# Kernel tuning notes

Hardware: AMD Instinct MI355X
Metric: run time of the kernel (lower is better)

Reference implementation:

```python
import jax, jax.numpy as jnp
import numpy as np

D = 64      # n_embd (== head_size in this module)
H = 8       # n_heads
B = 4
T = 2048    # seq len == block_size
EPS = 1e-5


def layernorm(x, g, b):
    mu = jnp.mean(x, axis=-1, keepdims=True)
    var = jnp.mean(jnp.square(x - mu), axis=-1, keepdims=True)
    return (x - mu) * jax.lax.rsqrt(var + EPS) * g + b


def setup_inputs() -> dict:
    key = jax.random.key(0)
    ks = jax.random.split(key, 16)
    s = 1.0 / np.sqrt(D)
    inp = {
        'inputs': jax.random.normal(ks[0], (B, T, D), jnp.float32),
        # per-head QKV linears: weight [H, D, D] (in, out), bias [H, D]
        'Wq': jax.random.uniform(ks[1], (H, D, D), jnp.float32, -s, s),
        'bq': jax.random.uniform(ks[2], (H, D), jnp.float32, -s, s),
        'Wk': jax.random.uniform(ks[3], (H, D, D), jnp.float32, -s, s),
        'bk': jax.random.uniform(ks[4], (H, D), jnp.float32, -s, s),
        'Wv': jax.random.uniform(ks[5], (H, D, D), jnp.float32, -s, s),
        'bv': jax.random.uniform(ks[6], (H, D), jnp.float32, -s, s),
        # projection: Linear(H*D -> D)
        'Wp': jax.random.uniform(ks[7], (H * D, D), jnp.float32, -1/np.sqrt(H*D), 1/np.sqrt(H*D)),
        'bp': jax.random.uniform(ks[8], (D,), jnp.float32, -1/np.sqrt(H*D), 1/np.sqrt(H*D)),
        # FFN: D -> 4D -> D
        'W1': jax.random.uniform(ks[9], (D, 4 * D), jnp.float32, -s, s),
        'b1': jax.random.uniform(ks[10], (4 * D,), jnp.float32, -s, s),
        'W2': jax.random.uniform(ks[11], (4 * D, D), jnp.float32, -1/np.sqrt(4*D), 1/np.sqrt(4*D)),
        'b2': jax.random.uniform(ks[12], (D,), jnp.float32, -1/np.sqrt(4*D), 1/np.sqrt(4*D)),
        'g1': jnp.ones((D,), jnp.float32), 'be1': jnp.zeros((D,), jnp.float32),
        'g2': jnp.ones((D,), jnp.float32), 'be2': jnp.zeros((D,), jnp.float32),
    }
    return inp


def reference(inputs, Wq, bq, Wk, bk, Wv, bv, Wp, bp, W1, b1, W2, b2, g1, be1, g2, be2):
    x = inputs
    # per-head full-width QKV: [H, B, T, D]
    q = jnp.einsum('btd,hde->hbte', x, Wq) + bq[:, None, None, :]
    k = jnp.einsum('btd,hde->hbte', x, Wk) + bk[:, None, None, :]
    v = jnp.einsum('btd,hde->hbte', x, Wv) + bv[:, None, None, :]
    # unscaled scores (module has no 1/sqrt(d) scaling)
    scores = jnp.einsum('hbte,hbse->hbts', q, k)  # [H, B, T, T]
    causal = jnp.tril(jnp.ones((T, T), bool))
    scores = jnp.where(causal, scores, -jnp.inf)
    attn = jax.nn.softmax(scores, axis=-1)
    out = jnp.einsum('hbts,hbse->hbte', attn, v)  # [H, B, T, D]
    # torch.cat over heads along last dim -> [B, T, H*D]
    cat = jnp.transpose(out, (1, 2, 0, 3)).reshape(B, T, H * D)
    attn_out = cat @ Wp + bp
    h1 = layernorm(x + attn_out, g1, be1)
    ffn = jax.nn.relu(h1 @ W1 + b1) @ W2 + b2
    return layernorm(h1 + ffn, g2, be2)
```

## Files before the change

### kernel.cpp

```cpp
#include <hip/hip_runtime.h>
#include <hip/hip_bf16.h>
#include <stdint.h>

#define Dd 64
#define Hh 8
#define Bb 4
#define Tt 2048
#define NT (Bb * Tt)

typedef __attribute__((ext_vector_type(4))) float f32x4;
typedef __attribute__((ext_vector_type(8))) __bf16 bf16x8;
typedef __attribute__((ext_vector_type(8))) uint16_t u16x8;

__device__ __forceinline__ uint16_t f2bf_fast(float f) {
    union { __bf16 h; uint16_t u; } c; c.h = (__bf16)f; return c.u;
}

#define SWZ(row, k)   ((row) * 72  + ((k) ^ ((((row) >> 3) & 7) << 3)))
#define PSZ(q, k)     ((q)  * 72  + ((k) ^ ((((q)  >> 2) & 3) << 3)))
#define W2SWZ(col, k) ((col) * 264 + ((k) ^ ((((col) >> 3) & 7) << 3)))
#define WPSWZ(col, k) ((col) * 520 + ((k) ^ ((((col) >> 3) & 7) << 3)))

__global__ __launch_bounds__(256) void qkv_kernel(
    const float* __restrict__ x,
    const float* __restrict__ Wq, const float* __restrict__ bq,
    const float* __restrict__ Wk, const float* __restrict__ bk,
    const float* __restrict__ Wv, const float* __restrict__ bv,
    uint16_t* __restrict__ qb, uint16_t* __restrict__ kb, uint16_t* __restrict__ vb)
{
    __shared__ uint16_t WtF[64 * 72];
    const int rt = blockIdx.x, h = blockIdx.y, m = blockIdx.z;
    const float* W    = (m == 0) ? Wq : (m == 1) ? Wk : Wv;
    const float* bias = (m == 0) ? bq : (m == 1) ? bk : bv;
    uint16_t*    out  = (m == 0) ? qb : (m == 1) ? kb : vb;
    const int t = threadIdx.x, lane = t & 63, w = t >> 6;
    const int l15 = lane & 15, g = lane >> 4;

#pragma unroll
    for (int p = 0; p < 4; ++p) {
        int idx = p * 256 + t;
        int r = idx >> 4, c4 = (idx & 15) * 4;
        f32x4 wv = *(const f32x4*)&W[(size_t)(h * 64 + r) * 64 + c4];
#pragma unroll
        for (int j = 0; j < 4; ++j) WtF[SWZ(c4 + j, r)] = f2bf_fast(wv[j]);
    }

    const int row = rt * 64 + w * 16 + l15;
    union { u16x8 u; bf16x8 b; } a0, a1;
    {
        f32x4 x0 = *(const f32x4*)&x[(size_t)row * 64 + g * 8];
        f32x4 x1 = *(const f32x4*)&x[(size_t)row * 64 + g * 8 + 4];
        f32x4 x2 = *(const f32x4*)&x[(size_t)row * 64 + 32 + g * 8];
        f32x4 x3 = *(const f32x4*)&x[(size_t)row * 64 + 32 + g * 8 + 4];
#pragma unroll
        for (int j = 0; j < 4; ++j) {
            a0.u[j] = f2bf_fast(x0[j]); a0.u[4 + j] = f2bf_fast(x1[j]);
            a1.u[j] = f2bf_fast(x2[j]); a1.u[4 + j] = f2bf_fast(x3[j]);
        }
    }
    __syncthreads();

    f32x4 acc[4] = {};
#pragma unroll
    for (int ct = 0; ct < 4; ++ct) {
        bf16x8 b0 = *(const bf16x8*)&WtF[SWZ(ct * 16 + l15, g * 8)];
        bf16x8 b1 = *(const bf16x8*)&WtF[SWZ(ct * 16 + l15, 32 + g * 8)];
        acc[ct] = __builtin_amdgcn_mfma_f32_16x16x32_bf16(a0.b, b0, acc[ct], 0, 0, 0);
        acc[ct] = __builtin_amdgcn_mfma_f32_16x16x32_bf16(a1.b, b1, acc[ct], 0, 0, 0);
    }
#pragma unroll
    for (int ct = 0; ct < 4; ++ct) {
        float bb = bias[h * 64 + ct * 16 + l15];
#pragma unroll
        for (int rr = 0; rr < 4; ++rr) {
            int orow = rt * 64 + w * 16 + g * 4 + rr;
            out[((size_t)h * NT + orow) * 64 + ct * 16 + l15] =
                f2bf_fast(acc[ct][rr] + bb);
        }
    }
}

__global__ __launch_bounds__(256) void attn_kernel3(
    const uint16_t* __restrict__ qb, const uint16_t* __restrict__ kb,
    const uint16_t* __restrict__ vb, uint16_t* __restrict__ cat)
{
    __shared__ uint16_t KsF[2][64 * 72];
    __shared__ uint16_t VtF[2][64 * 72];
    __shared__ uint16_t PsF[4][16 * 72];
    const int pairid = blockIdx.x, h = blockIdx.y, b = blockIdx.z;
    const int t = threadIdx.x, lane = t & 63, wave = t >> 6;
    const int l15 = lane & 15, g = lane >> 4;
    const size_t base = ((size_t)h * NT + (size_t)b * Tt) * 64;
    const uint16_t* Qh = qb + base;
    const uint16_t* Kh = kb + base;
    const uint16_t* Vh = vb + base;
    const int rS = t >> 3, cS = (t & 7) * 8;

    for (int ph = 0; ph < 2; ++ph) {
        const int qt = ph ? (31 - pairid) : pairid;
        bf16x8 aq0, aq1;
        {
            int qrow = qt * 64 + wave * 16 + l15;
            aq0 = *(const bf16x8*)&Qh[(size_t)qrow * 64 + g * 8];
            aq1 = *(const bf16x8*)&Qh[(size_t)qrow * 64 + 32 + g * 8];
        }
        f32x4 o[4] = {};
        float m_run[4], l_run[4];
#pragma unroll
        for (int r = 0; r < 4; ++r) { m_run[r] = -INFINITY; l_run[r] = 0.f; }

        __syncthreads();
        {
            u16x8 k0 = *(const u16x8*)&Kh[(size_t)(rS) * 64 + cS];
            u16x8 k1 = *(const u16x8*)&Kh[(size_t)(32 + rS) * 64 + cS];
            u16x8 v0 = *(const u16x8*)&Vh[(size_t)(rS) * 64 + cS];
            u16x8 v1 = *(const u16x8*)&Vh[(size_t)(32 + rS) * 64 + cS];
            *(u16x8*)&KsF[0][SWZ(rS, cS)] = k0;
            *(u16x8*)&KsF[0][SWZ(32 + rS, cS)] = k1;
#pragma unroll
            for (int j = 0; j < 8; ++j) {
                VtF[0][SWZ(cS + j, rS)] = v0[j];
                VtF[0][SWZ(cS + j, 32 + rS)] = v1[j];
            }
        }
        __syncthreads();

        for (int kv = 0; kv <= qt; ++kv) {
            const int cur = kv & 1;
            const bool pf = kv < qt;
            u16x8 pk0, pk1, pv0, pv1;
            if (pf) {
                int kr = (kv + 1) * 64;
                pk0 = *(const u16x8*)&Kh[(size_t)(kr + rS) * 64 + cS];
                pk1 = *(const u16x8*)&Kh[(size_t)(kr + 32 + rS) * 64 + cS];
                pv0 = *(const u16x8*)&Vh[(size_t)(kr + rS) * 64 + cS];
                pv1 = *(const u16x8*)&Vh[(size_t)(kr + 32 + rS) * 64 + cS];
            }
            f32x4 s[4];
#pragma unroll
            for (int kt = 0; kt < 4; ++kt) {
                bf16x8 bk0 = *(const bf16x8*)&KsF[cur][SWZ(kt * 16 + l15, g * 8)];
                bf16x8 bk1 = *(const bf16x8*)&KsF[cur][SWZ(kt * 16 + l15, 32 + g * 8)];
                f32x4 z = {};
                z = __builtin_amdgcn_mfma_f32_16x16x32_bf16(aq0, bk0, z, 0, 0, 0);
                z = __builtin_amdgcn_mfma_f32_16x16x32_bf16(aq1, bk1, z, 0, 0, 0);
                s[kt] = z;
            }
            if (kv == qt) {
#pragma unroll
                for (int kt = 0; kt < 4; ++kt) {
                    int key = kt * 16 + l15;
#pragma unroll
                    for (int r = 0; r < 4; ++r) {
                        int qr = wave * 16 + g * 4 + r;
                        if (key > qr) s[kt][r] = -INFINITY;
                    }
                }
            }
            float mt[4];
#pragma unroll
            for (int r = 0; r < 4; ++r) {
                mt[r] = fmaxf(fmaxf(s[0][r], s[1][r]), fmaxf(s[2][r], s[3][r]));
                mt[r] = fmaxf(mt[r], __shfl_xor(mt[r], 1));
                mt[r] = fmaxf(mt[r], __shfl_xor(mt[r], 2));
                mt[r] = fmaxf(mt[r], __shfl_xor(mt[r], 4));
                mt[r] = fmaxf(mt[r], __shfl_xor(mt[r], 8));
            }
            bool need = false;
#pragma unroll
            for (int r = 0; r < 4; ++r) need |= (mt[r] > m_run[r] + 8.f);
            if (__any((int)need)) {
#pragma unroll
                for (int r = 0; r < 4; ++r) {
                    float mnew = fmaxf(m_run[r], mt[r]);
                    float a = __expf(m_run[r] - mnew);
                    m_run[r] = mnew;
                    l_run[r] *= a;
                    o[0][r] *= a; o[1][r] *= a; o[2][r] *= a; o[3][r] *= a;
                }
            }
            float ls[4];
#pragma unroll
            for (int r = 0; r < 4; ++r) {
                float sum = 0.f;
#pragma unroll
                for (int kt = 0; kt < 4; ++kt) {
                    float p = __expf(s[kt][r] - m_run[r]);
                    s[kt][r] = p;
                    sum += p;
                }
                ls[r] = sum;
            }
#pragma unroll
            for (int r = 0; r < 4; ++r) {
                ls[r] += __shfl_xor(ls[r], 1);
                ls[r] += __shfl_xor(ls[r], 2);
                ls[r] += __shfl_xor(ls[r], 4);
                ls[r] += __shfl_xor(ls[r], 8);
                l_run[r] += ls[r];
            }
#pragma unroll
            for (int kt = 0; kt < 4; ++kt)
#pragma unroll
                for (int r = 0; r < 4; ++r)
                    PsF[wave][PSZ(g * 4 + r, kt * 16 + l15)] = f2bf_fast(s[kt][r]);
#pragma unroll
            for (int c = 0; c < 2; ++c) {
                bf16x8 ap = *(const bf16x8*)&PsF[wave][PSZ(l15, c * 32 + g * 8)];
#pragma unroll
                for (int dt = 0; dt < 4; ++dt) {
                    bf16x8 bv = *(const bf16x8*)&VtF[cur][SWZ(dt * 16 + l15, c * 32 + g * 8)];
                    o[dt] = __builtin_amdgcn_mfma_f32_16x16x32_bf16(ap, bv, o[dt], 0, 0, 0);
                }
            }
            if (pf) {
                *(u16x8*)&KsF[cur ^ 1][SWZ(rS, cS)] = pk0;
                *(u16x8*)&KsF[cur ^ 1][SWZ(32 + rS, cS)] = pk1;
#pragma unroll
                for (int j = 0; j < 8; ++j) {
                    VtF[cur ^ 1][SWZ(cS + j, rS)] = pv0[j];
                    VtF[cur ^ 1][SWZ(cS + j, 32 + rS)] = pv1[j];
                }
                __syncthreads();
            }
        }
        float inv[4];
#pragma unroll
        for (int r = 0; r < 4; ++r) inv[r] = 1.f / l_run[r];
#pragma unroll
        for (int dt = 0; dt < 4; ++dt)
#pragma unroll
            for (int r = 0; r < 4; ++r) {
                int row = qt * 64 + wave * 16 + g * 4 + r;
                cat[((size_t)b * Tt + row) * (Hh * 64) + h * 64 + dt * 16 + l15] =
                    f2bf_fast(o[dt][r] * inv[r]);
            }
    }
}

__global__ __launch_bounds__(256) void proj_ln1_mfma(
    const uint16_t* __restrict__ cat, const float* __restrict__ Wp,
    const float* __restrict__ bp, const float* __restrict__ x,
    const float* __restrict__ g1, const float* __restrict__ be1,
    float* __restrict__ h1, uint16_t* __restrict__ h1b)
{
    __shared__ uint16_t WptF[64 * 520];
    const int rt = blockIdx.x;
    const int t = threadIdx.x, lane = t & 63, w = t >> 6;
    const int l15 = lane & 15, g = lane >> 4;
#pragma unroll
    for (int p = 0; p < 32; ++p) {
        int idx = p * 256 + t;
        int r = idx >> 4, c4 = (idx & 15) * 4;
        f32x4 wv = *(const f32x4*)&Wp[(size_t)r * 64 + c4];
#pragma unroll
        for (int j = 0; j < 4; ++j) WptF[WPSWZ(c4 + j, r)] = f2bf_fast(wv[j]);
    }
    __syncthreads();
    const int arow = rt * 64 + w * 16 + l15;
    f32x4 acc[4] = {};
#pragma unroll
    for (int kt = 0; kt < 16; ++kt) {
        bf16x8 a = *(const bf16x8*)&cat[(size_t)arow * 512 + kt * 32 + g * 8];
#pragma unroll
        for (int ct = 0; ct < 4; ++ct) {
            bf16x8 bfr = *(const bf16x8*)&WptF[WPSWZ(ct * 16 + l15, kt * 32 + g * 8)];
            acc[ct] = __builtin_amdgcn_mfma_f32_16x16x32_bf16(a, bfr, acc[ct], 0, 0, 0);
        }
    }
    float bpv[4], g1v[4], b1v[4];
#pragma unroll
    for (int ct = 0; ct < 4; ++ct) {
        bpv[ct] = bp[ct * 16 + l15];
        g1v[ct] = g1[ct * 16 + l15];
        b1v[ct] = be1[ct * 16 + l15];
    }
#pragma unroll
    for (int rr = 0; rr < 4; ++rr) {
        int drow = rt * 64 + w * 16 + g * 4 + rr;
        float s[4], sum = 0.f;
#pragma unroll
        for (int ct = 0; ct < 4; ++ct) {
            s[ct] = acc[ct][rr] + bpv[ct] + x[(size_t)drow * 64 + ct * 16 + l15];
            sum += s[ct];
        }
        sum += __shfl_xor(sum, 1); sum += __shfl_xor(sum, 2);
        sum += __shfl_xor(sum, 4); sum += __shfl_xor(sum, 8);
        float mu = sum * (1.f / 64.f);
        float v = 0.f;
#pragma unroll
        for (int ct = 0; ct < 4; ++ct) { s[ct] -= mu; v += s[ct] * s[ct]; }
        v += __shfl_xor(v, 1); v += __shfl_xor(v, 2);
        v += __shfl_xor(v, 4); v += __shfl_xor(v, 8);
        float rstd = rsqrtf(v * (1.f / 64.f) + 1e-5f);
#pragma unroll
        for (int ct = 0; ct < 4; ++ct) {
            float hv = s[ct] * rstd * g1v[ct] + b1v[ct];
            h1 [(size_t)drow * 64 + ct * 16 + l15] = hv;
            h1b[(size_t)drow * 64 + ct * 16 + l15] = f2bf_fast(hv);
        }
    }
}

__global__ __launch_bounds__(256) void ffn_mfma(
    const uint16_t* __restrict__ h1b, const float* __restrict__ h1,
    const float* __restrict__ W1, const float* __restrict__ b1,
    const float* __restrict__ W2, const float* __restrict__ b2,
    const float* __restrict__ g2, const float* __restrict__ be2,
    float* __restrict__ out)
{
    __shared__ uint16_t W1t[256 * 72];
    __shared__ uint16_t W2t[64 * 264];
    __shared__ uint16_t hidS[4][16 * 264];
    const int rt = blockIdx.x;
    const int t = threadIdx.x, lane = t & 63, w = t >> 6;
    const int l15 = lane & 15, g = lane >> 4;
#pragma unroll
    for (int p = 0; p < 16; ++p) {
        int idx = p * 256 + t;
        int r = idx >> 6, c4 = (idx & 63) * 4;
        f32x4 wv = *(const f32x4*)&W1[(size_t)r * 256 + c4];
#pragma unroll
        for (int j = 0; j < 4; ++j) W1t[SWZ(c4 + j, r)] = f2bf_fast(wv[j]);
    }
#pragma unroll
    for (int p = 0; p < 16; ++p) {
        int idx = p * 256 + t;
        int r = idx >> 4, c4 = (idx & 15) * 4;
        f32x4 wv = *(const f32x4*)&W2[(size_t)r * 64 + c4];
#pragma unroll
        for (int j = 0; j < 4; ++j) W2t[W2SWZ(c4 + j, r)] = f2bf_fast(wv[j]);
    }
    __syncthreads();
    const int arow = rt * 64 + w * 16 + l15;
    f32x4 acc1[16] = {};
#pragma unroll
    for (int ks = 0; ks < 2; ++ks) {
        bf16x8 a = *(const bf16x8*)&h1b[(size_t)arow * 64 + ks * 32 + g * 8];
#pragma unroll
        for (int ct = 0; ct < 16; ++ct) {
            bf16x8 bfr = *(const bf16x8*)&W1t[SWZ(ct * 16 + l15, ks * 32 + g * 8)];
            acc1[ct] = __builtin_amdgcn_mfma_f32_16x16x32_bf16(a, bfr, acc1[ct], 0, 0, 0);
        }
    }
#pragma unroll
    for (int ct = 0; ct < 16; ++ct) {
        float bb = b1[ct * 16 + l15];
#pragma unroll
        for (int rr = 0; rr < 4; ++rr)
            hidS[w][(g * 4 + rr) * 264 + ct * 16 + l15] =
                f2bf_fast(fmaxf(acc1[ct][rr] + bb, 0.f));
    }
    f32x4 acc2[4] = {};
#pragma unroll
    for (int ks = 0; ks < 8; ++ks) {
        bf16x8 a = *(const bf16x8*)&hidS[w][l15 * 264 + ks * 32 + g * 8];
#pragma unroll
        for (int ct = 0; ct < 4; ++ct) {
            bf16x8 bfr = *(const bf16x8*)&W2t[W2SWZ(ct * 16 + l15, ks * 32 + g * 8)];
            acc2[ct] = __builtin_amdgcn_mfma_f32_16x16x32_bf16(a, bfr, acc2[ct], 0, 0, 0);
        }
    }
    float b2v[4], g2v[4], be2v[4];
#pragma unroll
    for (int ct = 0; ct < 4; ++ct) {
        b2v[ct]  = b2[ct * 16 + l15];
        g2v[ct]  = g2[ct * 16 + l15];
        be2v[ct] = be2[ct * 16 + l15];
    }
#pragma unroll
    for (int rr = 0; rr < 4; ++rr) {
        int drow = rt * 64 + w * 16 + g * 4 + rr;
        float s[4], sum = 0.f;
#pragma unroll
        for (int ct = 0; ct < 4; ++ct) {
            s[ct] = acc2[ct][rr] + b2v[ct] + h1[(size_t)drow * 64 + ct * 16 + l15];
            sum += s[ct];
        }
        sum += __shfl_xor(sum, 1); sum += __shfl_xor(sum, 2);
        sum += __shfl_xor(sum, 4); sum += __shfl_xor(sum, 8);
        float mu = sum * (1.f / 64.f);
        float v = 0.f;
#pragma unroll
        for (int ct = 0; ct < 4; ++ct) { s[ct] -= mu; v += s[ct] * s[ct]; }
        v += __shfl_xor(v, 1); v += __shfl_xor(v, 2);
        v += __shfl_xor(v, 4); v += __shfl_xor(v, 8);
        float rstd = rsqrtf(v * (1.f / 64.f) + 1e-5f);
#pragma unroll
        for (int ct = 0; ct < 4; ++ct)
            out[(size_t)drow * 64 + ct * 16 + l15] =
                s[ct] * rstd * g2v[ct] + be2v[ct];
    }
}

extern "C" void kernel_launch(void* const* d_in, const int* in_sizes, int n_in,
                              void* d_out, int out_size, void* d_ws, size_t ws_size,
                              hipStream_t stream)
{
    (void)in_sizes; (void)n_in; (void)out_size; (void)ws_size;
    const float* x   = (const float*)d_in[0];
    const float* Wq  = (const float*)d_in[1];
    const float* bq  = (const float*)d_in[2];
    const float* Wk  = (const float*)d_in[3];
    const float* bk  = (const float*)d_in[4];
    const float* Wv  = (const float*)d_in[5];
    const float* bv  = (const float*)d_in[6];
    const float* Wp  = (const float*)d_in[7];
    const float* bp  = (const float*)d_in[8];
    const float* W1  = (const float*)d_in[9];
    const float* b1  = (const float*)d_in[10];
    const float* W2  = (const float*)d_in[11];
    const float* b2  = (const float*)d_in[12];
    const float* g1  = (const float*)d_in[13];
    const float* be1 = (const float*)d_in[14];
    const float* g2  = (const float*)d_in[15];
    const float* be2 = (const float*)d_in[16];
    float* outp = (float*)d_out;

    char* w = (char*)d_ws;
    uint16_t* qb  = (uint16_t*)w;
    uint16_t* kb  = qb + (size_t)Hh * NT * 64;
    uint16_t* vb  = kb + (size_t)Hh * NT * 64;
    uint16_t* cat = vb + (size_t)Hh * NT * 64;
    float*    h1  = (float*)(cat + (size_t)NT * 512);
    uint16_t* h1b = (uint16_t*)(h1 + (size_t)NT * 64);

    qkv_kernel<<<dim3(NT / 64, Hh, 3), dim3(256), 0, stream>>>(
        x, Wq, bq, Wk, bk, Wv, bv, qb, kb, vb);
    attn_kernel3<<<dim3(16, Hh, Bb), dim3(256), 0, stream>>>(qb, kb, vb, cat);
    proj_ln1_mfma<<<dim3(NT / 64), dim3(256), 0, stream>>>(
        cat, Wp, bp, x, g1, be1, h1, h1b);
    ffn_mfma<<<dim3(NT / 64), dim3(256), 0, stream>>>(
        h1b, h1, W1, b1, W2, b2, g2, be2, outp);
}
```

Before: 192.2 us.

## Pre-convert weights and input to swizzled bf16 once; remap attention grid

Adds a setup kernel that converts x and all weight matrices to bf16 in their swizzled shared-memory layouts once per call. The qkv, projection and FFN kernels then copy those layouts straight into LDS instead of each block re-reading fp32 weights and converting them with scattered stores. The attention launch moves to a 1-D grid with a remapped block index, likely meant to spread heads and batches across XCDs for better L2 locality. This adds one extra kernel launch and extra workspace traffic.

```diff
diff --git a/kernel.cpp b/kernel.cpp
--- a/kernel.cpp
+++ b/kernel.cpp
@@ -21,43 +21,86 @@
 #define W2SWZ(col, k) ((col) * 264 + ((k) ^ ((((col) >> 3) & 7) << 3)))
 #define WPSWZ(col, k) ((col) * 520 + ((k) ^ ((((col) >> 3) & 7) << 3)))
 
+__global__ __launch_bounds__(256) void setup_kernel(
+    const float* __restrict__ x,
+    const float* __restrict__ Wq, const float* __restrict__ Wk,
+    const float* __restrict__ Wv, const float* __restrict__ Wp,
+    const float* __restrict__ W1, const float* __restrict__ W2,
+    uint16_t* __restrict__ xb, uint16_t* __restrict__ WtAll,
+    uint16_t* __restrict__ WptS, uint16_t* __restrict__ W1g,
+    uint16_t* __restrict__ W2g)
+{
+    const int bid = blockIdx.x, t = threadIdx.x;
+    if (bid < 256) {
+        size_t base = ((size_t)bid * 256 + t) * 8;
+        f32x4 a = *(const f32x4*)&x[base];
+        f32x4 b = *(const f32x4*)&x[base + 4];
+        u16x8 o;
+#pragma unroll
+        for (int j = 0; j < 4; ++j) { o[j] = f2bf_fast(a[j]); o[4 + j] = f2bf_fast(b[j]); }
+        *(u16x8*)&xb[base] = o;
+    } else if (bid < 280) {
+        const int mh = bid - 256, m = mh / 8, h = mh % 8;
+        const float* W = (m == 0) ? Wq : (m == 1) ? Wk : Wv;
+        uint16_t* dst = WtAll + (size_t)mh * 4608;
+#pragma unroll
+        for (int p = 0; p < 4; ++p) {
+            int idx = p * 256 + t;
+            int k = idx >> 4, c4 = (idx & 15) * 4;
+            f32x4 wv = *(const f32x4*)&W[(size_t)(h * 64 + k) * 64 + c4];
+#pragma unroll
+            for (int j = 0; j < 4; ++j) dst[SWZ(c4 + j, k)] = f2bf_fast(wv[j]);
+        }
+    } else if (bid < 288) {
+        const int j = bid - 280;
+#pragma unroll
+        for (int p = 0; p < 16; ++p) {
+            int idx = p * 256 + t;
+            int col = idx & 63, k = j * 64 + (idx >> 6);
+            WptS[WPSWZ(col, k)] = f2bf_fast(Wp[(size_t)k * 64 + col]);
+        }
+    } else if (bid < 292) {
+        const int j = bid - 288;
+#pragma unroll
+        for (int p = 0; p < 16; ++p) {
+            int e = j * 4096 + p * 256 + t;
+            int col = e & 255, k = e >> 8;
+            W1g[SWZ(col, k)] = f2bf_fast(W1[(size_t)k * 256 + col]);
+        }
+    } else {
+        const int j = bid - 292;
+#pragma unroll
+        for (int p = 0; p < 16; ++p) {
+            int e = j * 4096 + p * 256 + t;
+            int col = e & 63, k = e >> 6;
+            W2g[W2SWZ(col, k)] = f2bf_fast(W2[(size_t)k * 64 + col]);
+        }
+    }
+}
+
 __global__ __launch_bounds__(256) void qkv_kernel(
-    const float* __restrict__ x,
-    const float* __restrict__ Wq, const float* __restrict__ bq,
-    const float* __restrict__ Wk, const float* __restrict__ bk,
-    const float* __restrict__ Wv, const float* __restrict__ bv,
+    const uint16_t* __restrict__ xb, const uint16_t* __restrict__ WtAll,
+    const float* __restrict__ bq, const float* __restrict__ bk,
+    const float* __restrict__ bv,
     uint16_t* __restrict__ qb, uint16_t* __restrict__ kb, uint16_t* __restrict__ vb)
 {
     __shared__ uint16_t WtF[64 * 72];
     const int rt = blockIdx.x, h = blockIdx.y, m = blockIdx.z;
-    const float* W    = (m == 0) ? Wq : (m == 1) ? Wk : Wv;
     const float* bias = (m == 0) ? bq : (m == 1) ? bk : bv;
     uint16_t*    out  = (m == 0) ? qb : (m == 1) ? kb : vb;
     const int t = threadIdx.x, lane = t & 63, w = t >> 6;
     const int l15 = lane & 15, g = lane >> 4;
 
-#pragma unroll
-    for (int p = 0; p < 4; ++p) {
-        int idx = p * 256 + t;
-        int r = idx >> 4, c4 = (idx & 15) * 4;
-        f32x4 wv = *(const f32x4*)&W[(size_t)(h * 64 + r) * 64 + c4];
-#pragma unroll
-        for (int j = 0; j < 4; ++j) WtF[SWZ(c4 + j, r)] = f2bf_fast(wv[j]);
-    }
-
+    {
+        const u16x8* src = (const u16x8*)(WtAll + (size_t)(m * 8 + h) * 4608);
+        u16x8* dst = (u16x8*)WtF;
+        dst[t] = src[t];
+        dst[256 + t] = src[256 + t];
+        if (t < 64) dst[512 + t] = src[512 + t];
+    }
     const int row = rt * 64 + w * 16 + l15;
-    union { u16x8 u; bf16x8 b; } a0, a1;
-    {
-        f32x4 x0 = *(const f32x4*)&x[(size_t)row * 64 + g * 8];
-        f32x4 x1 = *(const f32x4*)&x[(size_t)row * 64 + g * 8 + 4];
-        f32x4 x2 = *(const f32x4*)&x[(size_t)row * 64 + 32 + g * 8];
-        f32x4 x3 = *(const f32x4*)&x[(size_t)row * 64 + 32 + g * 8 + 4];
-#pragma unroll
-        for (int j = 0; j < 4; ++j) {
-            a0.u[j] = f2bf_fast(x0[j]); a0.u[4 + j] = f2bf_fast(x1[j]);
-            a1.u[j] = f2bf_fast(x2[j]); a1.u[4 + j] = f2bf_fast(x3[j]);
-        }
-    }
+    bf16x8 a0 = *(const bf16x8*)&xb[(size_t)row * 64 + g * 8];
+    bf16x8 a1 = *(const bf16x8*)&xb[(size_t)row * 64 + 32 + g * 8];
     __syncthreads();
 
     f32x4 acc[4] = {};
@@ -65,8 +108,8 @@
     for (int ct = 0; ct < 4; ++ct) {
         bf16x8 b0 = *(const bf16x8*)&WtF[SWZ(ct * 16 + l15, g * 8)];
         bf16x8 b1 = *(const bf16x8*)&WtF[SWZ(ct * 16 + l15, 32 + g * 8)];
-        acc[ct] = __builtin_amdgcn_mfma_f32_16x16x32_bf16(a0.b, b0, acc[ct], 0, 0, 0);
-        acc[ct] = __builtin_amdgcn_mfma_f32_16x16x32_bf16(a1.b, b1, acc[ct], 0, 0, 0);
+        acc[ct] = __builtin_amdgcn_mfma_f32_16x16x32_bf16(a0, b0, acc[ct], 0, 0, 0);
+        acc[ct] = __builtin_amdgcn_mfma_f32_16x16x32_bf16(a1, b1, acc[ct], 0, 0, 0);
     }
 #pragma unroll
     for (int ct = 0; ct < 4; ++ct) {
@@ -80,14 +123,18 @@
     }
 }
 
-__global__ __launch_bounds__(256) void attn_kernel3(
+__global__ __launch_bounds__(256) void attn_kernel4(
     const uint16_t* __restrict__ qb, const uint16_t* __restrict__ kb,
     const uint16_t* __restrict__ vb, uint16_t* __restrict__ cat)
 {
     __shared__ uint16_t KsF[2][64 * 72];
     __shared__ uint16_t VtF[2][64 * 72];
     __shared__ uint16_t PsF[4][16 * 72];
-    const int pairid = blockIdx.x, h = blockIdx.y, b = blockIdx.z;
+    const int bid = blockIdx.x;
+    const int lbid = (bid & 7) * 64 + (bid >> 3);
+    const int pairid = lbid & 15;
+    const int hb = lbid >> 4;
+    const int h = hb & 7, b = hb >> 3;
     const int t = threadIdx.x, lane = t & 63, wave = t >> 6;
     const int l15 = lane & 15, g = lane >> 4;
     const size_t base = ((size_t)h * NT + (size_t)b * Tt) * 64;
@@ -239,7 +286,7 @@
 }
 
 __global__ __launch_bounds__(256) void proj_ln1_mfma(
-    const uint16_t* __restrict__ cat, const float* __restrict__ Wp,
+    const uint16_t* __restrict__ cat, const uint16_t* __restrict__ WptS,
     const float* __restrict__ bp, const float* __restrict__ x,
     const float* __restrict__ g1, const float* __restrict__ be1,
     float* __restrict__ h1, uint16_t* __restrict__ h1b)
@@ -248,13 +295,12 @@
     const int rt = blockIdx.x;
     const int t = threadIdx.x, lane = t & 63, w = t >> 6;
     const int l15 = lane & 15, g = lane >> 4;
-#pragma unroll
-    for (int p = 0; p < 32; ++p) {
-        int idx = p * 256 + t;
-        int r = idx >> 4, c4 = (idx & 15) * 4;
-        f32x4 wv = *(const f32x4*)&Wp[(size_t)r * 64 + c4];
-#pragma unroll
-        for (int j = 0; j < 4; ++j) WptF[WPSWZ(c4 + j, r)] = f2bf_fast(wv[j]);
+    {
+        const u16x8* src = (const u16x8*)WptS;
+        u16x8* dst = (u16x8*)WptF;
+#pragma unroll
+        for (int p = 0; p < 16; ++p) dst[p * 256 + t] = src[p * 256 + t];
+        if (t < 64) dst[4096 + t] = src[4096 + t];
     }
     __syncthreads();
     const int arow = rt * 64 + w * 16 + l15;
@@ -304,32 +350,27 @@
 
 __global__ __launch_bounds__(256) void ffn_mfma(
     const uint16_t* __restrict__ h1b, const float* __restrict__ h1,
-    const float* __restrict__ W1, const float* __restrict__ b1,
-    const float* __restrict__ W2, const float* __restrict__ b2,
+    const uint16_t* __restrict__ w1g, const float* __restrict__ b1,
+    const uint16_t* __restrict__ w2g, const float* __restrict__ b2,
     const float* __restrict__ g2, const float* __restrict__ be2,
     float* __restrict__ out)
 {
-    __shared__ uint16_t W1t[256 * 72];
-    __shared__ uint16_t W2t[64 * 264];
+    __shared__ uint16_t W1s[256 * 72];
+    __shared__ uint16_t W2s[64 * 264];
     __shared__ uint16_t hidS[4][16 * 264];
     const int rt = blockIdx.x;
     const int t = threadIdx.x, lane = t & 63, w = t >> 6;
     const int l15 = lane & 15, g = lane >> 4;
-#pragma unroll
-    for (int p = 0; p < 16; ++p) {
-        int idx = p * 256 + t;
-        int r = idx >> 6, c4 = (idx & 63) * 4;
-        f32x4 wv = *(const f32x4*)&W1[(size_t)r * 256 + c4];
-#pragma unroll
-        for (int j = 0; j < 4; ++j) W1t[SWZ(c4 + j, r)] = f2bf_fast(wv[j]);
-    }
-#pragma unroll
-    for (int p = 0; p < 16; ++p) {
-        int idx = p * 256 + t;
-        int r = idx >> 4, c4 = (idx & 15) * 4;
-        f32x4 wv = *(const f32x4*)&W2[(size_t)r * 64 + c4];
-#pragma unroll
-        for (int j = 0; j < 4; ++j) W2t[W2SWZ(c4 + j, r)] = f2bf_fast(wv[j]);
+    {
+        const u16x8* s1 = (const u16x8*)w1g;
+        u16x8* d1 = (u16x8*)W1s;
+#pragma unroll
+        for (int p = 0; p < 9; ++p) d1[p * 256 + t] = s1[p * 256 + t];
+        const u16x8* s2 = (const u16x8*)w2g;
+        u16x8* d2 = (u16x8*)W2s;
+#pragma unroll
+        for (int p = 0; p < 8; ++p) d2[p * 256 + t] = s2[p * 256 + t];
+        if (t < 64) d2[2048 + t] = s2[2048 + t];
     }
     __syncthreads();
     const int arow = rt * 64 + w * 16 + l15;
@@ -339,7 +380,7 @@
         bf16x8 a = *(const bf16x8*)&h1b[(size_t)arow * 64 + ks * 32 + g * 8];
 #pragma unroll
         for (int ct = 0; ct < 16; ++ct) {
-            bf16x8 bfr = *(const bf16x8*)&W1t[SWZ(ct * 16 + l15, ks * 32 + g * 8)];
+            bf16x8 bfr = *(const bf16x8*)&W1s[SWZ(ct * 16 + l15, ks * 32 + g * 8)];
             acc1[ct] = __builtin_amdgcn_mfma_f32_16x16x32_bf16(a, bfr, acc1[ct], 0, 0, 0);
         }
     }
@@ -357,7 +398,7 @@
         bf16x8 a = *(const bf16x8*)&hidS[w][l15 * 264 + ks * 32 + g * 8];
 #pragma unroll
         for (int ct = 0; ct < 4; ++ct) {
-            bf16x8 bfr = *(const bf16x8*)&W2t[W2SWZ(ct * 16 + l15, ks * 32 + g * 8)];
+            bf16x8 bfr = *(const bf16x8*)&W2s[W2SWZ(ct * 16 + l15, ks * 32 + g * 8)];
             acc2[ct] = __builtin_amdgcn_mfma_f32_16x16x32_bf16(a, bfr, acc2[ct], 0, 0, 0);
         }
     }
@@ -418,18 +459,25 @@
     float* outp = (float*)d_out;
 
     char* w = (char*)d_ws;
-    uint16_t* qb  = (uint16_t*)w;
-    uint16_t* kb  = qb + (size_t)Hh * NT * 64;
-    uint16_t* vb  = kb + (size_t)Hh * NT * 64;
-    uint16_t* cat = vb + (size_t)Hh * NT * 64;
-    float*    h1  = (float*)(cat + (size_t)NT * 512);
-    uint16_t* h1b = (uint16_t*)(h1 + (size_t)NT * 64);
-
+    uint16_t* qb   = (uint16_t*)w;
+    uint16_t* kb   = qb + (size_t)Hh * NT * 64;
+    uint16_t* vb   = kb + (size_t)Hh * NT * 64;
+    uint16_t* cat  = vb + (size_t)Hh * NT * 64;
+    float*    h1   = (float*)(cat + (size_t)NT * 512);
+    uint16_t* h1b  = (uint16_t*)(h1 + (size_t)NT * 64);
+    uint16_t* xb   = h1b + (size_t)NT * 64;
+    uint16_t* WtAll= xb + (size_t)NT * 64;
+    uint16_t* WptS = WtAll + (size_t)24 * 4608;
+    uint16_t* W1g  = WptS + 33280;
+    uint16_t* W2g  = W1g + 18432;
+
+    setup_kernel<<<dim3(296), dim3(256), 0, stream>>>(
+        x, Wq, Wk, Wv, Wp, W1, W2, xb, WtAll, WptS, W1g, W2g);
     qkv_kernel<<<dim3(NT / 64, Hh, 3), dim3(256), 0, stream>>>(
-        x, Wq, bq, Wk, bk, Wv, bv, qb, kb, vb);
-    attn_kernel3<<<dim3(16, Hh, Bb), dim3(256), 0, stream>>>(qb, kb, vb, cat);
+        xb, WtAll, bq, bk, bv, qb, kb, vb);
+    attn_kernel4<<<dim3(512), dim3(256), 0, stream>>>(qb, kb, vb, cat);
     proj_ln1_mfma<<<dim3(NT / 64), dim3(256), 0, stream>>>(
-        cat, Wp, bp, x, g1, be1, h1, h1b);
+        cat, WptS, bp, x, g1, be1, h1, h1b);
     ffn_mfma<<<dim3(NT / 64), dim3(256), 0, stream>>>(
-        h1b, h1, W1, b1, W2, b2, g2, be2, outp);
-}
+        h1b, h1, W1g, b1, W2g, b2, g2, be2, outp);
+}
```

Result: faster. 185.3 us (-3.6%).
